# Optimization experiments

Measured on AMD Instinct MI355X. Metric: run time of the kernel, lower is better.

## Reference

```python
import jax, jax.numpy as jnp
import numpy as np

EMBED_DIM = 1024
NUM_HEADS = 16
PROJ_DIM = EMBED_DIM // NUM_HEADS


def setup_inputs() -> dict:
    key = jax.random.key(0)
    ks = jax.random.split(key, 11)
    B, S, D = 2, 2048, EMBED_DIM
    scale = 1.0 / np.sqrt(D)
    inp = {
        'q': jax.random.normal(ks[0], (B, S, D), jnp.float32),
        'k': jax.random.normal(ks[1], (B, S, D), jnp.float32),
        'v': jax.random.normal(ks[2], (B, S, D), jnp.float32),
        'Wq': jax.random.normal(ks[3], (D, D), jnp.float32) * scale,
        'bq': jnp.zeros((D,), jnp.float32),
        'Wk': jax.random.normal(ks[4], (D, D), jnp.float32) * scale,
        'bk': jnp.zeros((D,), jnp.float32),
        'Wv': jax.random.normal(ks[5], (D, D), jnp.float32) * scale,
        'bv': jnp.zeros((D,), jnp.float32),
        'Wo': jax.random.normal(ks[6], (D, D), jnp.float32) * scale,
        'bo': jnp.zeros((D,), jnp.float32),
        'use_causal_mask': 1,
    }
    return inp


def _split_heads(x, B):
    # [B, S, D] -> [B, H, S, Pd]
    return x.reshape(B, -1, NUM_HEADS, PROJ_DIM).transpose(0, 2, 1, 3)


def reference(q, k, v, Wq, bq, Wk, bk, Wv, bv, Wo, bo, use_causal_mask):
    B, S, D = q.shape
    qh = _split_heads(q @ Wq + bq, B)
    kh = _split_heads(k @ Wk + bk, B)
    vh = _split_heads(v @ Wv + bv, B)
    # scaled dot-product attention; scores [B, H, S, S]
    logits = jnp.einsum('bhqd,bhkd->bhqk', qh, kh) / jnp.sqrt(
        jnp.asarray(PROJ_DIM, jnp.float32))
    if use_causal_mask:
        # faithful to source: logits += log(tril * 1e-9 + 1e-9)
        tril = jnp.tril(jnp.ones((S, S), dtype=logits.dtype))
        logits = logits + jnp.log(tril * 1e-9 + 1e-9)
    attn = jax.nn.softmax(logits, axis=-1)
    out = jnp.einsum('bhqk,bhkd->bhqd', attn, vh)
    out = out.transpose(0, 2, 1, 3).reshape(B, S, D)
    return out @ Wo + bo
```

## Files before the change

kernel.cpp:

```cpp
#include <hip/hip_runtime.h>
#include <hip/hip_bf16.h>
#include <stdint.h>

#define EMBED 1024
#define NH    16
#define PD    64
#define BATCH 2
#define SEQ   2048

typedef unsigned short u16;
typedef __attribute__((ext_vector_type(8))) short bf16x8;
typedef __attribute__((ext_vector_type(4))) float f32x4;

#define WAITALL() __builtin_amdgcn_s_waitcnt(0)

__device__ __forceinline__ float b2f(u16 x) {
  unsigned u = ((unsigned)x) << 16;
  return __builtin_bit_cast(float, u);
}
__device__ __forceinline__ u16 cvtb(float x) {
  __bf16 h = (__bf16)x;
  return __builtin_bit_cast(u16, h);
}
__device__ __forceinline__ float loadIn(const void* p, size_t i, int isf32) {
  return isf32 ? ((const float*)p)[i] : b2f(((const u16*)p)[i]);
}
__device__ __forceinline__ void async16(const void* g, void* l) {
  __builtin_amdgcn_global_load_lds((const __attribute__((address_space(1))) void*)g,
                                   (__attribute__((address_space(3))) void*)l,
                                   16, 0, 0);
}

__global__ void detect(const unsigned* q, int* flag) {
  int lane = threadIdx.x;
  unsigned lo = q[lane] & 0xffffu;
  unsigned e = (lo >> 7) & 0xffu;
  int pred = (e >= 110 && e <= 135);
  unsigned long long m = __ballot(pred);
  if (lane == 0) flag[0] = (__popcll(m) < 32) ? 1 : 0;
}

__global__ __launch_bounds__(256) void conv_qkv(const void* q, const void* k,
                                                const void* v, u16* qb, u16* kb,
                                                u16* vb, const int* flag) {
  const int isf32 = flag[0];
  size_t i = ((size_t)blockIdx.x * 256 + threadIdx.x) * 8;
  const void* src = (blockIdx.y == 0) ? q : (blockIdx.y == 1) ? k : v;
  u16* dst = (blockIdx.y == 0) ? qb : (blockIdx.y == 1) ? kb : vb;
  u16 tmp[8];
  if (isf32) {
    const float* s = (const float*)src + i;
    float4 a = *(const float4*)s;
    float4 b = *(const float4*)(s + 4);
    tmp[0] = cvtb(a.x); tmp[1] = cvtb(a.y); tmp[2] = cvtb(a.z); tmp[3] = cvtb(a.w);
    tmp[4] = cvtb(b.x); tmp[5] = cvtb(b.y); tmp[6] = cvtb(b.z); tmp[7] = cvtb(b.w);
  } else {
    const uint4 r = *(const uint4*)((const u16*)src + i);
    *(uint4*)tmp = r;
  }
  *(uint4*)(dst + i) = *(uint4*)tmp;
}

__global__ __launch_bounds__(256) void conv_w(const void* Wq, const void* Wk,
                                              const void* Wv, const void* Wo,
                                              u16* out, const int* flag) {
  const int isf32 = flag[0];
  const void* W = (blockIdx.z == 0) ? Wq : (blockIdx.z == 1) ? Wk
                : (blockIdx.z == 2) ? Wv : Wo;
  u16* WT = out + (size_t)blockIdx.z * EMBED * EMBED;
  __shared__ float sh[64][65];
  int r0 = blockIdx.y * 64, c0 = blockIdx.x * 64;
  int col = threadIdx.x & 63;
  int rb  = threadIdx.x >> 6;
#pragma unroll
  for (int i = 0; i < 16; i++) {
    int row = i * 4 + rb;
    sh[row][col] = loadIn(W, (size_t)(r0 + row) * EMBED + c0 + col, isf32);
  }
  __syncthreads();
#pragma unroll
  for (int i = 0; i < 16; i++) {
    int row = i * 4 + rb;
    WT[(size_t)(c0 + row) * EMBED + r0 + col] = cvtb(sh[col][row]);
  }
}

__device__ __forceinline__ void gemm_core(const u16* __restrict__ A,
                                          const u16* __restrict__ Bt,
                                          int tm, int tn, u16* lds,
                                          f32x4 acc[4][4]) {
  const int tid = threadIdx.x;
  const int lane = tid & 63;
  const int wv = tid >> 6;
  const int wm = (wv >> 1) * 64, wn = (wv & 1) * 64;
  const int l15 = lane & 15, quad = lane >> 4;
  const int rbx = (lane & 7) << 3;
  u16* As = lds;
  u16* Bs = lds + 128 * 64;
  f32x4 z = {0.f, 0.f, 0.f, 0.f};
#pragma unroll
  for (int i = 0; i < 4; i++)
#pragma unroll
    for (int j = 0; j < 4; j++) acc[i][j] = z;

  for (int kt = 0; kt < EMBED; kt += 64) {
#pragma unroll
    for (int i = 0; i < 4; i++) {
      int c = i * 256 + tid;
      int row = c >> 3;
      int col = ((c & 7) << 3) ^ ((row & 7) << 3);
      async16(A + (size_t)(tm + row) * EMBED + kt + col, As + c * 8);
      async16(Bt + (size_t)(tn + row) * EMBED + kt + col, Bs + c * 8);
    }
    WAITALL();
    __syncthreads();
#pragma unroll
    for (int ks = 0; ks < 64; ks += 32) {
      int ko = (ks + quad * 8) ^ rbx;
      bf16x8 af[4], bf[4];
#pragma unroll
      for (int mt = 0; mt < 4; mt++)
        af[mt] = *(const bf16x8*)(As + (wm + mt * 16 + l15) * 64 + ko);
#pragma unroll
      for (int nt = 0; nt < 4; nt++)
        bf[nt] = *(const bf16x8*)(Bs + (wn + nt * 16 + l15) * 64 + ko);
#pragma unroll
      for (int mt = 0; mt < 4; mt++)
#pragma unroll
        for (int nt = 0; nt < 4; nt++)
          acc[mt][nt] = __builtin_amdgcn_mfma_f32_16x16x32_bf16(
              af[mt], bf[nt], acc[mt][nt], 0, 0, 0);
    }
    WAITALL();
    __syncthreads();
  }
}

__global__ __launch_bounds__(256) void qkv_gemm(
    const u16* qb, const u16* kb, const u16* vb, const u16* wts,
    const void* bq, const void* bk, const void* bv,
    u16* Qh, u16* Kh, u16* Vt, const int* flag) {
  __shared__ __align__(16) u16 lds[2 * 128 * 64];
  const int isf32 = flag[0];
  int z = blockIdx.z;
  const u16* A = (z == 0) ? qb : (z == 1) ? kb : vb;
  const u16* Bt = wts + (size_t)z * EMBED * EMBED;
  const void* bias = (z == 0) ? bq : (z == 1) ? bk : bv;
  int tm = blockIdx.y * 128, tn = blockIdx.x * 128;
  f32x4 acc[4][4];
  gemm_core(A, Bt, tm, tn, lds, acc);

  int lane = threadIdx.x & 63, wv = threadIdx.x >> 6;
  int wm = (wv >> 1) * 64, wn = (wv & 1) * 64;
  int rbase = tm + wm + ((lane >> 4) << 2);
  int cbase = tn + wn + (lane & 15);
  if (z < 2) {
    u16* dst = (z == 0) ? Qh : Kh;
#pragma unroll
    for (int mt = 0; mt < 4; mt++)
#pragma unroll
      for (int nt = 0; nt < 4; nt++) {
        int col = cbase + nt * 16;
        float bv_ = loadIn(bias, col, isf32);
        int h = col >> 6, p = col & 63;
#pragma unroll
        for (int j = 0; j < 4; j++) {
          int row = rbase + mt * 16 + j;
          int b = row >> 11, s = row & 2047;
          dst[(((size_t)(b * NH + h) * SEQ) + s) * PD + p] =
              cvtb(acc[mt][nt][j] + bv_);
        }
      }
  } else {
#pragma unroll
    for (int mt = 0; mt < 4; mt++)
#pragma unroll
      for (int nt = 0; nt < 4; nt++) {
        int col = cbase + nt * 16;
        float bv_ = loadIn(bias, col, isf32);
        int h = col >> 6, p = col & 63;
        int row0 = rbase + mt * 16;
        int b = row0 >> 11, s0 = row0 & 2047;
        int beta = s0 >> 5, w = s0 & 31;
        int pos = (beta << 5) + (((w >> 2) & 3) << 3) + ((w >> 4) << 2);
        ushort4 pk;
        pk.x = cvtb(acc[mt][nt][0] + bv_);
        pk.y = cvtb(acc[mt][nt][1] + bv_);
        pk.z = cvtb(acc[mt][nt][2] + bv_);
        pk.w = cvtb(acc[mt][nt][3] + bv_);
        *(ushort4*)(Vt + ((size_t)(b * NH + h) * PD + p) * SEQ + pos) = pk;
      }
  }
}

__global__ __launch_bounds__(256) void attn(const u16* __restrict__ Qh,
                                            const u16* __restrict__ Kh,
                                            const u16* __restrict__ Vt,
                                            u16* __restrict__ O,
                                            const int* __restrict__ maskflag) {
  __shared__ __align__(16) u16 Qs[128 * 64];
  __shared__ __align__(16) u16 Ks[64 * 64];
  __shared__ __align__(16) u16 Vs[64 * 64];
  const int bh = blockIdx.y;
  const int qt = blockIdx.x * 128;
  const int tid = threadIdx.x, lane = tid & 63, wv = tid >> 6;
  const int l15 = lane & 15, quad = lane >> 4;
  const int rbx = (lane & 7) << 3;
  const size_t head = (size_t)bh * SEQ * PD;
  const bool causal = (maskflag[0] != 0);
  const float C = 0.18033688011112042f;

#pragma unroll
  for (int i = 0; i < 4; i++) {
    int c = i * 256 + tid;
    int row = c >> 3;
    int col = ((c & 7) << 3) ^ ((row & 7) << 3);
    async16(Qh + head + (size_t)(qt + row) * PD + col, Qs + c * 8);
  }
  WAITALL();
  __syncthreads();
  bf16x8 qf[2][2];
#pragma unroll
  for (int ks = 0; ks < 2; ks++) {
    int ko = (ks * 32 + quad * 8) ^ rbx;
    qf[ks][0] = *(const bf16x8*)(Qs + (wv * 32 + l15) * 64 + ko);
    qf[ks][1] = *(const bf16x8*)(Qs + (wv * 32 + 16 + l15) * 64 + ko);
  }

  float lacc[2] = {0.f, 0.f};
  f32x4 oacc[4][2];
  f32x4 z4 = {0.f, 0.f, 0.f, 0.f};
#pragma unroll
  for (int mt = 0; mt < 4; mt++)
#pragma unroll
    for (int n = 0; n < 2; n++) oacc[mt][n] = z4;

  const int rowq = qt + wv * 32;

  for (int t = 0; t < SEQ / 64; t++) {
    const int k0 = t * 64;
#pragma unroll
    for (int i = 0; i < 2; i++) {
      int c = i * 256 + tid;
      int row = c >> 3;
      int col = ((c & 7) << 3) ^ ((row & 7) << 3);
      async16(Kh + head + (size_t)(k0 + row) * PD + col, Ks + c * 8);
      async16(Vt + head + (size_t)row * SEQ + k0 + col, Vs + c * 8);
    }
    WAITALL();
    __syncthreads();

    f32x4 st[4][2];
#pragma unroll
    for (int kt = 0; kt < 4; kt++)
#pragma unroll
      for (int n = 0; n < 2; n++) st[kt][n] = z4;
#pragma unroll
    for (int ks = 0; ks < 2; ks++) {
      int ko = (ks * 32 + quad * 8) ^ rbx;
#pragma unroll
      for (int kt = 0; kt < 4; kt++) {
        bf16x8 kf = *(const bf16x8*)(Ks + (kt * 16 + l15) * 64 + ko);
        st[kt][0] = __builtin_amdgcn_mfma_f32_16x16x32_bf16(kf, qf[ks][0], st[kt][0], 0, 0, 0);
        st[kt][1] = __builtin_amdgcn_mfma_f32_16x16x32_bf16(kf, qf[ks][1], st[kt][1], 0, 0, 0);
      }
    }

    const int mode = !causal ? 0 : (k0 > qt + 127 ? 2 : (k0 + 63 <= qt ? 0 : 1));
    const float ub = (mode == 2) ? -17.f : -16.f;
    unsigned pw[2][2][4];
#pragma unroll
    for (int kt = 0; kt < 4; kt++) {
#pragma unroll
      for (int n = 0; n < 2; n++) {
        const int qrow = rowq + n * 16 + l15;
        float p[4];
#pragma unroll
        for (int r = 0; r < 4; r++) {
          float bias = ub;
          if (mode == 1) {
            int kappa = k0 + kt * 16 + 4 * quad + r;
            bias = (kappa > qrow) ? -17.f : -16.f;
          }
          p[r] = exp2f(fmaf(st[kt][n][r], C, bias));
        }
        lacc[n] += (p[0] + p[1]) + (p[2] + p[3]);
        pw[kt >> 1][n][(kt & 1) * 2 + 0] =
            (unsigned)cvtb(p[0]) | ((unsigned)cvtb(p[1]) << 16);
        pw[kt >> 1][n][(kt & 1) * 2 + 1] =
            (unsigned)cvtb(p[2]) | ((unsigned)cvtb(p[3]) << 16);
      }
    }

#pragma unroll
    for (int p = 0; p < 2; p++) {
      bf16x8 pf[2];
      pf[0] = __builtin_bit_cast(bf16x8,
          (uint4){pw[p][0][0], pw[p][0][1], pw[p][0][2], pw[p][0][3]});
      pf[1] = __builtin_bit_cast(bf16x8,
          (uint4){pw[p][1][0], pw[p][1][1], pw[p][1][2], pw[p][1][3]});
#pragma unroll
      for (int mt = 0; mt < 4; mt++) {
        int row = mt * 16 + l15;
        int chunk = ((p << 2) + quad) ^ (row & 7);
        bf16x8 vf = *(const bf16x8*)(Vs + row * 64 + (chunk << 3));
        oacc[mt][0] = __builtin_amdgcn_mfma_f32_16x16x32_bf16(vf, pf[0], oacc[mt][0], 0, 0, 0);
        oacc[mt][1] = __builtin_amdgcn_mfma_f32_16x16x32_bf16(vf, pf[1], oacc[mt][1], 0, 0, 0);
      }
    }
    WAITALL();
    __syncthreads();
  }

#pragma unroll
  for (int n = 0; n < 2; n++) {
    lacc[n] += __shfl_xor(lacc[n], 16, 64);
    lacc[n] += __shfl_xor(lacc[n], 32, 64);
  }
  float inv[2] = {1.f / lacc[0], 1.f / lacc[1]};

  const int b = bh >> 4, h = bh & 15;
#pragma unroll
  for (int mt = 0; mt < 4; mt++) {
#pragma unroll
    for (int n = 0; n < 2; n++) {
      int qrow = rowq + n * 16 + l15;
      ushort4 w;
      w.x = cvtb(oacc[mt][n][0] * inv[n]);
      w.y = cvtb(oacc[mt][n][1] * inv[n]);
      w.z = cvtb(oacc[mt][n][2] * inv[n]);
      w.w = cvtb(oacc[mt][n][3] * inv[n]);
      *(ushort4*)(O + ((size_t)b * SEQ + qrow) * EMBED + h * PD + mt * 16 +
                  4 * quad) = w;
    }
  }
}

__global__ __launch_bounds__(256) void out_gemm(const u16* __restrict__ Ob,
                                                const u16* __restrict__ WoT,
                                                const void* __restrict__ bo,
                                                void* __restrict__ out,
                                                const int* __restrict__ flag) {
  __shared__ __align__(16) u16 lds[2 * 128 * 64];
  const int isf32 = flag[0];
  int tm = blockIdx.y * 128, tn = blockIdx.x * 128;
  f32x4 acc[4][4];
  gemm_core(Ob, WoT, tm, tn, lds, acc);
  int lane = threadIdx.x & 63, wv = threadIdx.x >> 6;
  int wm = (wv >> 1) * 64, wn = (wv & 1) * 64;
  int rbase = tm + wm + ((lane >> 4) << 2);
  int cbase = tn + wn + (lane & 15);
#pragma unroll
  for (int mt = 0; mt < 4; mt++)
#pragma unroll
    for (int nt = 0; nt < 4; nt++) {
      int col = cbase + nt * 16;
      float bv_ = loadIn(bo, col, isf32);
#pragma unroll
      for (int j = 0; j < 4; j++) {
        int row = rbase + mt * 16 + j;
        float val = acc[mt][nt][j] + bv_;
        size_t off = (size_t)row * EMBED + col;
        if (isf32) ((float*)out)[off] = val;
        else       ((u16*)out)[off]   = cvtb(val);
      }
    }
}

extern "C" void kernel_launch(void* const* d_in, const int* in_sizes, int n_in,
                              void* d_out, int out_size, void* d_ws, size_t ws_size,
                              hipStream_t stream) {
  const void* q  = d_in[0];
  const void* k  = d_in[1];
  const void* v  = d_in[2];
  const void* Wq = d_in[3];
  const void* bq = d_in[4];
  const void* Wk = d_in[5];
  const void* bk = d_in[6];
  const void* Wv = d_in[7];
  const void* bv = d_in[8];
  const void* Wo = d_in[9];
  const void* bo = d_in[10];
  const int* msk = (const int*)d_in[11];

  char* ws = (char*)d_ws;
  int*  flag  = (int*)ws;
  u16*  qb    = (u16*)(ws + 64);
  u16*  kb    = qb + (size_t)4194304;
  u16*  vb    = kb + (size_t)4194304;
  u16*  WT    = vb + (size_t)4194304;
  u16*  Qh    = WT + (size_t)4194304;
  u16*  Kh    = Qh + (size_t)4194304;
  u16*  Vt    = Kh + (size_t)4194304;
  u16*  Ob    = Vt + (size_t)4194304;

  detect<<<1, 64, 0, stream>>>((const unsigned*)q, flag);
  conv_qkv<<<dim3(2048, 3), 256, 0, stream>>>(q, k, v, qb, kb, vb, flag);
  conv_w<<<dim3(16, 16, 4), 256, 0, stream>>>(Wq, Wk, Wv, Wo, WT, flag);
  qkv_gemm<<<dim3(8, 32, 3), 256, 0, stream>>>(qb, kb, vb, WT, bq, bk, bv,
                                               Qh, Kh, Vt, flag);
  attn<<<dim3(16, 32), 256, 0, stream>>>(Qh, Kh, Vt, Ob, msk);
  out_gemm<<<dim3(8, 32), 256, 0, stream>>>(Ob, WT + (size_t)3 * 1048576,
                                            bo, d_out, flag);
}
```

Before: 307.5 us.

## Double-buffer K/V tiles in attention and LDS stages in output GEMM

The attention kernel now keeps two K/V shared-memory buffers and issues the async loads for the next key tile before computing on the current one, so global-to-LDS transfer can overlap the MFMA and softmax work. The output projection GEMM gets the same two-stage prefetch, doubling its LDS. The QKV GEMM is only refactored into stage and compute helpers and stays single-buffered, dropping one redundant wait. The larger LDS footprint may lower occupancy. The attention loop also has no barrier between the next-tile prefetch and the current compute, so the overwrite of the previous buffer and the cross-wave visibility of the newly loaded tile rely on the barrier that remains at the end of the loop.

```diff
diff --git a/kernel.cpp b/kernel.cpp
--- a/kernel.cpp
+++ b/kernel.cpp
@@ -85,54 +85,39 @@
   }
 }
 
-__device__ __forceinline__ void gemm_core(const u16* __restrict__ A,
-                                          const u16* __restrict__ Bt,
-                                          int tm, int tn, u16* lds,
-                                          f32x4 acc[4][4]) {
-  const int tid = threadIdx.x;
-  const int lane = tid & 63;
-  const int wv = tid >> 6;
-  const int wm = (wv >> 1) * 64, wn = (wv & 1) * 64;
-  const int l15 = lane & 15, quad = lane >> 4;
-  const int rbx = (lane & 7) << 3;
-  u16* As = lds;
-  u16* Bs = lds + 128 * 64;
-  f32x4 z = {0.f, 0.f, 0.f, 0.f};
-#pragma unroll
-  for (int i = 0; i < 4; i++)
-#pragma unroll
-    for (int j = 0; j < 4; j++) acc[i][j] = z;
-
-  for (int kt = 0; kt < EMBED; kt += 64) {
-#pragma unroll
-    for (int i = 0; i < 4; i++) {
-      int c = i * 256 + tid;
-      int row = c >> 3;
-      int col = ((c & 7) << 3) ^ ((row & 7) << 3);
-      async16(A + (size_t)(tm + row) * EMBED + kt + col, As + c * 8);
-      async16(Bt + (size_t)(tn + row) * EMBED + kt + col, Bs + c * 8);
-    }
-    WAITALL();
-    __syncthreads();
-#pragma unroll
-    for (int ks = 0; ks < 64; ks += 32) {
-      int ko = (ks + quad * 8) ^ rbx;
-      bf16x8 af[4], bf[4];
-#pragma unroll
-      for (int mt = 0; mt < 4; mt++)
-        af[mt] = *(const bf16x8*)(As + (wm + mt * 16 + l15) * 64 + ko);
+__device__ __forceinline__ void gemm_stage(const u16* __restrict__ A,
+                                           const u16* __restrict__ Bt,
+                                           int tm, int tn, int kt,
+                                           u16* As, u16* Bs, int tid) {
+#pragma unroll
+  for (int i = 0; i < 4; i++) {
+    int c = i * 256 + tid;
+    int row = c >> 3;
+    int col = ((c & 7) << 3) ^ ((row & 7) << 3);
+    async16(A + (size_t)(tm + row) * EMBED + kt + col, As + c * 8);
+    async16(Bt + (size_t)(tn + row) * EMBED + kt + col, Bs + c * 8);
+  }
+}
+
+__device__ __forceinline__ void gemm_compute(const u16* As, const u16* Bs,
+                                             int wm, int wn, int l15, int quad,
+                                             int rbx, f32x4 acc[4][4]) {
+#pragma unroll
+  for (int ks = 0; ks < 64; ks += 32) {
+    int ko = (ks + quad * 8) ^ rbx;
+    bf16x8 af[4], bf[4];
+#pragma unroll
+    for (int mt = 0; mt < 4; mt++)
+      af[mt] = *(const bf16x8*)(As + (wm + mt * 16 + l15) * 64 + ko);
+#pragma unroll
+    for (int nt = 0; nt < 4; nt++)
+      bf[nt] = *(const bf16x8*)(Bs + (wn + nt * 16 + l15) * 64 + ko);
+#pragma unroll
+    for (int mt = 0; mt < 4; mt++)
 #pragma unroll
       for (int nt = 0; nt < 4; nt++)
-        bf[nt] = *(const bf16x8*)(Bs + (wn + nt * 16 + l15) * 64 + ko);
-#pragma unroll
-      for (int mt = 0; mt < 4; mt++)
-#pragma unroll
-        for (int nt = 0; nt < 4; nt++)
-          acc[mt][nt] = __builtin_amdgcn_mfma_f32_16x16x32_bf16(
-              af[mt], bf[nt], acc[mt][nt], 0, 0, 0);
-    }
-    WAITALL();
-    __syncthreads();
+        acc[mt][nt] = __builtin_amdgcn_mfma_f32_16x16x32_bf16(
+            af[mt], bf[nt], acc[mt][nt], 0, 0, 0);
   }
 }
 
@@ -147,13 +132,28 @@
   const u16* Bt = wts + (size_t)z * EMBED * EMBED;
   const void* bias = (z == 0) ? bq : (z == 1) ? bk : bv;
   int tm = blockIdx.y * 128, tn = blockIdx.x * 128;
+
+  const int tid = threadIdx.x, lane = tid & 63, wv = tid >> 6;
+  const int wm = (wv >> 1) * 64, wn = (wv & 1) * 64;
+  const int l15 = lane & 15, quad = lane >> 4;
+  const int rbx = (lane & 7) << 3;
   f32x4 acc[4][4];
-  gemm_core(A, Bt, tm, tn, lds, acc);
-
-  int lane = threadIdx.x & 63, wv = threadIdx.x >> 6;
-  int wm = (wv >> 1) * 64, wn = (wv & 1) * 64;
-  int rbase = tm + wm + ((lane >> 4) << 2);
-  int cbase = tn + wn + (lane & 15);
+  f32x4 zz = {0.f, 0.f, 0.f, 0.f};
+#pragma unroll
+  for (int i = 0; i < 4; i++)
+#pragma unroll
+    for (int j = 0; j < 4; j++) acc[i][j] = zz;
+
+  for (int kt = 0; kt < EMBED; kt += 64) {
+    gemm_stage(A, Bt, tm, tn, kt, lds, lds + 8192, tid);
+    WAITALL();
+    __syncthreads();
+    gemm_compute(lds, lds + 8192, wm, wn, l15, quad, rbx, acc);
+    __syncthreads();
+  }
+
+  int rbase = tm + wm + (quad << 2);
+  int cbase = tn + wn + l15;
   if (z < 2) {
     u16* dst = (z == 0) ? Qh : Kh;
 #pragma unroll
@@ -199,8 +199,8 @@
                                             u16* __restrict__ O,
                                             const int* __restrict__ maskflag) {
   __shared__ __align__(16) u16 Qs[128 * 64];
-  __shared__ __align__(16) u16 Ks[64 * 64];
-  __shared__ __align__(16) u16 Vs[64 * 64];
+  __shared__ __align__(16) u16 Ks[2][64 * 64];
+  __shared__ __align__(16) u16 Vs[2][64 * 64];
   const int bh = blockIdx.y;
   const int qt = blockIdx.x * 128;
   const int tid = threadIdx.x, lane = tid & 63, wv = tid >> 6;
@@ -210,6 +210,11 @@
   const bool causal = (maskflag[0] != 0);
   const float C = 0.18033688011112042f;
 
+  const int c0 = tid, c1 = 256 + tid;
+  const int r0 = c0 >> 3, r1 = c1 >> 3;
+  const int x0 = ((c0 & 7) << 3) ^ ((r0 & 7) << 3);
+  const int x1 = ((c1 & 7) << 3) ^ ((r1 & 7) << 3);
+
 #pragma unroll
   for (int i = 0; i < 4; i++) {
     int c = i * 256 + tid;
@@ -217,8 +222,13 @@
     int col = ((c & 7) << 3) ^ ((row & 7) << 3);
     async16(Qh + head + (size_t)(qt + row) * PD + col, Qs + c * 8);
   }
+  async16(Kh + head + (size_t)r0 * PD + x0, Ks[0] + c0 * 8);
+  async16(Kh + head + (size_t)r1 * PD + x1, Ks[0] + c1 * 8);
+  async16(Vt + head + (size_t)r0 * SEQ + x0, Vs[0] + c0 * 8);
+  async16(Vt + head + (size_t)r1 * SEQ + x1, Vs[0] + c1 * 8);
   WAITALL();
   __syncthreads();
+
   bf16x8 qf[2][2];
 #pragma unroll
   for (int ks = 0; ks < 2; ks++) {
@@ -239,16 +249,18 @@
 
   for (int t = 0; t < SEQ / 64; t++) {
     const int k0 = t * 64;
-#pragma unroll
-    for (int i = 0; i < 2; i++) {
-      int c = i * 256 + tid;
-      int row = c >> 3;
-      int col = ((c & 7) << 3) ^ ((row & 7) << 3);
-      async16(Kh + head + (size_t)(k0 + row) * PD + col, Ks + c * 8);
-      async16(Vt + head + (size_t)row * SEQ + k0 + col, Vs + c * 8);
-    }
-    WAITALL();
-    __syncthreads();
+    const int cur = t & 1;
+    if (t + 1 < SEQ / 64) {
+      const int kn = k0 + 64;
+      u16* Kn = Ks[cur ^ 1];
+      u16* Vn = Vs[cur ^ 1];
+      async16(Kh + head + (size_t)(kn + r0) * PD + x0, Kn + c0 * 8);
+      async16(Kh + head + (size_t)(kn + r1) * PD + x1, Kn + c1 * 8);
+      async16(Vt + head + (size_t)r0 * SEQ + kn + x0, Vn + c0 * 8);
+      async16(Vt + head + (size_t)r1 * SEQ + kn + x1, Vn + c1 * 8);
+    }
+    const u16* Ksc = Ks[cur];
+    const u16* Vsc = Vs[cur];
 
     f32x4 st[4][2];
 #pragma unroll
@@ -260,7 +272,7 @@
       int ko = (ks * 32 + quad * 8) ^ rbx;
 #pragma unroll
       for (int kt = 0; kt < 4; kt++) {
-        bf16x8 kf = *(const bf16x8*)(Ks + (kt * 16 + l15) * 64 + ko);
+        bf16x8 kf = *(const bf16x8*)(Ksc + (kt * 16 + l15) * 64 + ko);
         st[kt][0] = __builtin_amdgcn_mfma_f32_16x16x32_bf16(kf, qf[ks][0], st[kt][0], 0, 0, 0);
         st[kt][1] = __builtin_amdgcn_mfma_f32_16x16x32_bf16(kf, qf[ks][1], st[kt][1], 0, 0, 0);
       }
@@ -303,7 +315,7 @@
       for (int mt = 0; mt < 4; mt++) {
         int row = mt * 16 + l15;
         int chunk = ((p << 2) + quad) ^ (row & 7);
-        bf16x8 vf = *(const bf16x8*)(Vs + row * 64 + (chunk << 3));
+        bf16x8 vf = *(const bf16x8*)(Vsc + row * 64 + (chunk << 3));
         oacc[mt][0] = __builtin_amdgcn_mfma_f32_16x16x32_bf16(vf, pf[0], oacc[mt][0], 0, 0, 0);
         oacc[mt][1] = __builtin_amdgcn_mfma_f32_16x16x32_bf16(vf, pf[1], oacc[mt][1], 0, 0, 0);
       }
@@ -341,15 +353,36 @@
                                                 const void* __restrict__ bo,
                                                 void* __restrict__ out,
                                                 const int* __restrict__ flag) {
-  __shared__ __align__(16) u16 lds[2 * 128 * 64];
+  __shared__ __align__(16) u16 lds[4 * 128 * 64];
   const int isf32 = flag[0];
   int tm = blockIdx.y * 128, tn = blockIdx.x * 128;
+  const int tid = threadIdx.x, lane = tid & 63, wv = tid >> 6;
+  const int wm = (wv >> 1) * 64, wn = (wv & 1) * 64;
+  const int l15 = lane & 15, quad = lane >> 4;
+  const int rbx = (lane & 7) << 3;
   f32x4 acc[4][4];
-  gemm_core(Ob, WoT, tm, tn, lds, acc);
-  int lane = threadIdx.x & 63, wv = threadIdx.x >> 6;
-  int wm = (wv >> 1) * 64, wn = (wv & 1) * 64;
-  int rbase = tm + wm + ((lane >> 4) << 2);
-  int cbase = tn + wn + (lane & 15);
+  f32x4 zz = {0.f, 0.f, 0.f, 0.f};
+#pragma unroll
+  for (int i = 0; i < 4; i++)
+#pragma unroll
+    for (int j = 0; j < 4; j++) acc[i][j] = zz;
+
+  gemm_stage(Ob, WoT, tm, tn, 0, lds, lds + 8192, tid);
+  WAITALL();
+  __syncthreads();
+  for (int kt = 0; kt < EMBED; kt += 64) {
+    const int cur = (kt >> 6) & 1;
+    u16* curb = lds + cur * 16384;
+    if (kt + 64 < EMBED)
+      gemm_stage(Ob, WoT, tm, tn, kt + 64, lds + (cur ^ 1) * 16384,
+                 lds + (cur ^ 1) * 16384 + 8192, tid);
+    gemm_compute(curb, curb + 8192, wm, wn, l15, quad, rbx, acc);
+    WAITALL();
+    __syncthreads();
+  }
+
+  int rbase = tm + wm + (quad << 2);
+  int cbase = tn + wn + l15;
 #pragma unroll
   for (int mt = 0; mt < 4; mt++)
 #pragma unroll
```

Result: faster. 296.7 us (-3.5%).
